# Performance work log

Hardware: AMD Instinct MI355X
Metric: run time of the kernel (lower is better)

## Reference

```python
import jax, jax.numpy as jnp
import numpy as np

NX, NY = 4096, 4096


def setup_inputs() -> dict:
    key = jax.random.key(0)
    k1, k2 = jax.random.split(key)
    u_main = jax.random.normal(k1, (NX, NY), dtype=jnp.float32)
    u_coupled = jax.random.normal(k2, (NX, NY), dtype=jnp.float32)
    D_eff = jnp.array([0.05], dtype=jnp.float32)
    dirichlet_val = jnp.array([1.0, 0.0, 1.0, 0.0], dtype=jnp.float32)
    stencil = jnp.array([1.0, -1.0], dtype=jnp.float32)  # fixed [1,-1] stencil
    return {
        "u_main": u_main,
        "u_coupled": u_coupled,
        "D_eff": D_eff,
        "dirichlet_val": dirichlet_val,
        "stencil": stencil,
        "t": 1,
    }


def reference(u_main, u_coupled, D_eff, dirichlet_val, stencil, t):
    # Flux_Kernels.forward with Dirichlet BCs on all four boundaries and
    # is_retardation_a_func=False (ret_inv = ones), so u_coupled and t are unused.
    D = D_eff[0]
    s0, s1 = stencil[0], stencil[1]
    ret = jnp.ones_like(u_main)  # ret_inv when no retardation function

    # left (x- direction): boundary row 0, neighbors rows 1..Nx-1
    left_bound = ((s0 * dirichlet_val[0] + s1 * u_main[0, :]) * D * ret[0, :])[None, :]
    left_nb = (s0 * u_main[:-1, :] + s1 * u_main[1:, :]) * D * ret[1:, :]
    left_flux = jnp.concatenate([left_bound, left_nb], axis=0)

    # right (x+ direction): neighbors rows 0..Nx-2, boundary row Nx-1
    right_bound = ((s0 * dirichlet_val[1] + s1 * u_main[-1, :]) * D * ret[-1, :])[None, :]
    right_nb = (s0 * u_main[1:, :] + s1 * u_main[:-1, :]) * D * ret[:-1, :]
    right_flux = jnp.concatenate([right_nb, right_bound], axis=0)

    # top (y- direction): boundary col 0, neighbors cols 1..Ny-1
    top_bound = ((s0 * dirichlet_val[2] + s1 * u_main[:, 0]) * D * ret[:, 0])[:, None]
    top_nb = (s0 * u_main[:, :-1] + s1 * u_main[:, 1:]) * D * ret[:, 1:]
    top_flux = jnp.concatenate([top_bound, top_nb], axis=1)

    # bottom (y+ direction): neighbors cols 0..Ny-2, boundary col Ny-1
    bottom_bound = ((s0 * dirichlet_val[3] + s1 * u_main[:, -1]) * D * ret[:, -1])[:, None]
    bottom_nb = (s0 * u_main[:, 1:] + s1 * u_main[:, :-1]) * D * ret[:, :-1]
    bottom_flux = jnp.concatenate([bottom_nb, bottom_bound], axis=1)

    return left_flux + right_flux + top_flux + bottom_flux
```

## Files before the change

### kernel.cpp

```cpp
#include <hip/hip_runtime.h>
#include <cstdint>


#define NX 4096
#define NY 4096
#define TR 32
#define HR (TR + 2)
#define TC 256
#define LSTRIDE 264
#define HOFF (HR * LSTRIDE)
#define BUF_FLOATS (HOFF + 128)
#define CHUNKS 4

typedef float float4v __attribute__((ext_vector_type(4)));

__device__ __forceinline__ void row_to_lds(const float* g, float* l) {
    __builtin_amdgcn_global_load_lds(
        (const __attribute__((address_space(1))) uint32_t*)g,
        (__attribute__((address_space(3))) uint32_t*)l, 16, 0, 0);
}
__device__ __forceinline__ void sc_to_lds(const float* g, float* l) {
    __builtin_amdgcn_global_load_lds(
        (const __attribute__((address_space(1))) uint32_t*)g,
        (__attribute__((address_space(3))) uint32_t*)l, 4, 0, 0);
}

#define WAIT_VM(NSTR) { asm volatile("s_waitcnt vmcnt(" NSTR ")" ::: "memory"); \
                        __builtin_amdgcn_sched_barrier(0); }
#define WAIT_LGKM0    { asm volatile("s_waitcnt lgkmcnt(0)" ::: "memory");      \
                        __builtin_amdgcn_sched_barrier(0); }
#define BAR           __builtin_amdgcn_s_barrier();

__global__ __launch_bounds__(256, 2) void flux_stencil_kernel(
    const float* __restrict__ u,
    const float* __restrict__ D_eff,
    const float* __restrict__ dv,
    const float* __restrict__ st,
    float* __restrict__ out)
{
    __shared__ float s[2][BUF_FLOATS];

    const float D  = D_eff[0];
    const float s0 = st[0];
    const float s1 = st[1];
    const float k1 = D * s0;
    const float k4 = 4.0f * D * s1;
    const float dvUp = dv[0], dvDn = dv[1], dvL = dv[2], dvR = dv[3];

    const int b    = blockIdx.x;
    const int X    = b & 7;
    const int r    = b >> 3;
    const int ct   = r & 15;
    const int band = X * 4 + (r >> 4);
    const int j0   = ct * TC;
    const int i0b  = band * (TR * CHUNKS);

    const int t    = threadIdx.x;
    const int w    = t >> 6;
    const int lane = t & 63;

    const bool lEdgeCol = (j0 == 0);
    const bool rEdgeCol = (j0 + TC == NY);

    #define STAGE(m)                                                           \
    {                                                                          \
        float* sb = s[(m) & 1];                                                \
        const int i0 = i0b + (m) * TR;                                         \
        for (int k = w; k < HR; k += 4) {                    \
            int gr = i0 + k - 1;                                               \
            gr = gr < 0 ? 0 : (gr > NX - 1 ? NX - 1 : gr);                     \
            row_to_lds(u + (size_t)gr * NY + j0 + 4 * lane, sb + k * LSTRIDE); \
        }                                                                      \
        if (w == 2) {                                       \
            const int gr  = i0 + (lane < TR ? lane : TR - 1);                  \
            const int col = lEdgeCol ? 0 : j0 - 1;                             \
            sc_to_lds(u + (size_t)gr * NY + col, sb + HOFF);                   \
        }                                                                      \
        if (w == 3) {                                      \
            const int gr  = i0 + (lane < TR ? lane : TR - 1);                  \
            const int col = rEdgeCol ? NY - 1 : j0 + TC;                       \
            sc_to_lds(u + (size_t)gr * NY + col, sb + HOFF + 64);              \
        }                                                                      \
    }

    #define COMPUTE(m)                                                         \
    {                                                                          \
        const float* sb = s[(m) & 1];                                          \
        const int i0 = i0b + (m) * TR;                                         \
        const bool topE = (band == 0)  && ((m) == 0);                          \
        const bool botE = (band == 31) && ((m) == CHUNKS - 1);                 \
        const int cOff = 4 * lane;                                             \
        const int lOff = (lane == 0) ? 0 : cOff - 4;                           \
        const int rOff = cOff + 4;                  \
        _Pragma("unroll")                                                      \
        for (int rr8 = 0; rr8 < 8; ++rr8) {                                    \
            const int rr = w * 8 + rr8;               \
            const int k  = rr + 1;                                             \
            const float* rowc = sb + k * LSTRIDE;                              \
            float4v up = *(const float4v*)(sb + (k - 1) * LSTRIDE + cOff);     \
            float4v c  = *(const float4v*)(rowc + cOff);                       \
            float4v dn = *(const float4v*)(sb + (k + 1) * LSTRIDE + cOff);     \
            const float4v lv = *(const float4v*)(rowc + lOff);                 \
            const float4v rv = *(const float4v*)(rowc + rOff);                 \
            const float hl = sb[HOFF + rr];                \
            const float hr = sb[HOFF + 64 + rr];                               \
            const float lft = (lane == 0)  ? (lEdgeCol ? dvL : hl) : lv.w;     \
            const float rgt = (lane == 63) ? (rEdgeCol ? dvR : hr) : rv.x;     \
            if (topE && rr == 0)      { up.x=dvUp; up.y=dvUp; up.z=dvUp; up.w=dvUp; } \
            if (botE && rr == TR - 1) { dn.x=dvDn; dn.y=dvDn; dn.z=dvDn; dn.w=dvDn; } \
            float4v o;                                                         \
            o.x = k1 * (up.x + dn.x + lft + c.y) + k4 * c.x;                   \
            o.y = k1 * (up.y + dn.y + c.x + c.z) + k4 * c.y;                   \
            o.z = k1 * (up.z + dn.z + c.y + c.w) + k4 * c.z;                   \
            o.w = k1 * (up.w + dn.w + c.z + rgt) + k4 * c.w;                   \
            *(float4v*)(out + (size_t)(i0 + rr) * NY + j0 + cOff) = o;         \
        }                                                                      \
    }

    STAGE(0)
    STAGE(1)
    WAIT_VM("9")  BAR
    COMPUTE(0)
    WAIT_LGKM0    BAR
    STAGE(2)
    WAIT_VM("17") BAR
    COMPUTE(1)
    WAIT_LGKM0    BAR
    STAGE(3)
    WAIT_VM("17") BAR
    COMPUTE(2)
    WAIT_VM("8")  BAR
    COMPUTE(3)

    #undef STAGE
    #undef COMPUTE
}

extern "C" void kernel_launch(void* const* d_in, const int* in_sizes, int n_in,
                              void* d_out, int out_size, void* d_ws, size_t ws_size,
                              hipStream_t stream) {
    const float* u_main    = (const float*)d_in[0];
    const float* D_eff     = (const float*)d_in[2];
    const float* dirichlet = (const float*)d_in[3];
    const float* stencil   = (const float*)d_in[4];
    float* outp = (float*)d_out;

    const int grid  = 512;
    const int block = 256;

    flux_stencil_kernel<<<grid, block, 0, stream>>>(u_main, D_eff, dirichlet, stencil, outp);
}
```

Measured before the change: 26.55 us.

## Halve row tile, double grid, and reuse stencil rows in registers

Row tile height drops from 32 to 16 and the grid doubles to 1024 blocks. Occupancy hint rises to 4 blocks per CU, and the smaller LDS footprint allows that. The compute loop now keeps the up and centre rows in registers and loads only the next row each iteration, cutting redundant LDS reads. The cost is a larger halo fraction, since 18 staged rows serve 16 output rows, plus retuned vmcnt waits that must match the new load counts.

```diff
diff --git a/kernel.cpp b/kernel.cpp
--- a/kernel.cpp
+++ b/kernel.cpp
@@ -4,7 +4,7 @@
 
 #define NX 4096
 #define NY 4096
-#define TR 32
+#define TR 16
 #define HR (TR + 2)
 #define TC 256
 #define LSTRIDE 264
@@ -31,7 +31,7 @@
                         __builtin_amdgcn_sched_barrier(0); }
 #define BAR           __builtin_amdgcn_s_barrier();
 
-__global__ __launch_bounds__(256, 2) void flux_stencil_kernel(
+__global__ __launch_bounds__(256, 4) void flux_stencil_kernel(
     const float* __restrict__ u,
     const float* __restrict__ D_eff,
     const float* __restrict__ dv,
@@ -51,7 +51,7 @@
     const int X    = b & 7;
     const int r    = b >> 3;
     const int ct   = r & 15;
-    const int band = X * 4 + (r >> 4);
+    const int band = X * 8 + (r >> 4);
     const int j0   = ct * TC;
     const int i0b  = band * (TR * CHUNKS);
 
@@ -88,25 +88,27 @@
         const float* sb = s[(m) & 1];                                          \
         const int i0 = i0b + (m) * TR;                                         \
         const bool topE = (band == 0)  && ((m) == 0);                          \
-        const bool botE = (band == 31) && ((m) == CHUNKS - 1);                 \
+        const bool botE = (band == 63) && ((m) == CHUNKS - 1);                 \
         const int cOff = 4 * lane;                                             \
-        const int lOff = (lane == 0) ? 0 : cOff - 4;                           \
-        const int rOff = cOff + 4;                  \
+        const int lOff = (lane == 0) ? 0 : cOff - 4;         \
+        const int rOff = cOff + 4;                            \
+        const int rrB  = w * 4;                         \
+        const int kB   = rrB + 1;                             \
+        float4v up = *(const float4v*)(sb + (kB - 1) * LSTRIDE + cOff);        \
+        float4v c  = *(const float4v*)(sb + kB * LSTRIDE + cOff);              \
+        const float4v lv0 = *(const float4v*)(sb + kB * LSTRIDE + lOff);       \
+        const float4v rv0 = *(const float4v*)(sb + kB * LSTRIDE + rOff);       \
+        float lft = (lane == 0)  ? (lEdgeCol ? dvL : sb[HOFF + rrB])      : lv0.w; \
+        float rgt = (lane == 63) ? (rEdgeCol ? dvR : sb[HOFF + 64 + rrB]) : rv0.x; \
+        if (topE && w == 0) { up.x = dvUp; up.y = dvUp; up.z = dvUp; up.w = dvUp; } \
         _Pragma("unroll")                                                      \
-        for (int rr8 = 0; rr8 < 8; ++rr8) {                                    \
-            const int rr = w * 8 + rr8;               \
+        for (int rr4 = 0; rr4 < 4; ++rr4) {                                    \
+            const int rr = rrB + rr4;                        \
             const int k  = rr + 1;                                             \
-            const float* rowc = sb + k * LSTRIDE;                              \
-            float4v up = *(const float4v*)(sb + (k - 1) * LSTRIDE + cOff);     \
-            float4v c  = *(const float4v*)(rowc + cOff);                       \
-            float4v dn = *(const float4v*)(sb + (k + 1) * LSTRIDE + cOff);     \
-            const float4v lv = *(const float4v*)(rowc + lOff);                 \
-            const float4v rv = *(const float4v*)(rowc + rOff);                 \
-            const float hl = sb[HOFF + rr];                \
-            const float hr = sb[HOFF + 64 + rr];                               \
-            const float lft = (lane == 0)  ? (lEdgeCol ? dvL : hl) : lv.w;     \
-            const float rgt = (lane == 63) ? (rEdgeCol ? dvR : hr) : rv.x;     \
-            if (topE && rr == 0)      { up.x=dvUp; up.y=dvUp; up.z=dvUp; up.w=dvUp; } \
+            const float* nrow = sb + (k + 1) * LSTRIDE;                        \
+            float4v dn        = *(const float4v*)(nrow + cOff);                \
+            const float4v dnl = *(const float4v*)(nrow + lOff);                \
+            const float4v dnr = *(const float4v*)(nrow + rOff);                \
             if (botE && rr == TR - 1) { dn.x=dvDn; dn.y=dvDn; dn.z=dvDn; dn.w=dvDn; } \
             float4v o;                                                         \
             o.x = k1 * (up.x + dn.x + lft + c.y) + k4 * c.x;                   \
@@ -114,22 +116,26 @@
             o.z = k1 * (up.z + dn.z + c.y + c.w) + k4 * c.z;                   \
             o.w = k1 * (up.w + dn.w + c.z + rgt) + k4 * c.w;                   \
             *(float4v*)(out + (size_t)(i0 + rr) * NY + j0 + cOff) = o;         \
+            up  = c;                                                           \
+            c   = dn;                                                          \
+            lft = (lane == 0)  ? (lEdgeCol ? dvL : sb[HOFF + rr + 1])      : dnl.w; \
+            rgt = (lane == 63) ? (rEdgeCol ? dvR : sb[HOFF + 64 + rr + 1]) : dnr.x; \
         }                                                                      \
     }
 
     STAGE(0)
     STAGE(1)
-    WAIT_VM("9")  BAR
+    WAIT_VM("5")  BAR
     COMPUTE(0)
     WAIT_LGKM0    BAR
     STAGE(2)
-    WAIT_VM("17") BAR
+    WAIT_VM("9")  BAR
     COMPUTE(1)
     WAIT_LGKM0    BAR
     STAGE(3)
-    WAIT_VM("17") BAR
+    WAIT_VM("9")  BAR
     COMPUTE(2)
-    WAIT_VM("8")  BAR
+    WAIT_VM("4")  BAR
     COMPUTE(3)
 
     #undef STAGE
@@ -145,7 +151,7 @@
     const float* stencil   = (const float*)d_in[4];
     float* outp = (float*)d_out;
 
-    const int grid  = 512;
+    const int grid  = 1024;
     const int block = 256;
 
     flux_stencil_kernel<<<grid, block, 0, stream>>>(u_main, D_eff, dirichlet, stencil, outp);
```

Result: faster. 25.52 us (-3.9%).
